# Kernel tuning notes

Hardware: AMD Instinct MI355X
Metric: run time of the kernel (lower is better)

The kernel has to match this reference:

```python
import jax, jax.numpy as jnp
import numpy as np

NUM_KEYS = 8192
NUM_BINS = 128
NUM_FREQS = 64
NUM_KERNELS = 3
HEAD_DIM = 2 * NUM_FREQS


def setup_inputs() -> dict:
    key = jax.random.key(0)
    k1, k2, k3, k4, k5 = jax.random.split(key, 5)
    fan_in = NUM_FREQS * NUM_KERNELS
    bound = np.sqrt(6.0 / fan_in)
    return {
        "K": jax.random.normal(k1, (NUM_KEYS, HEAD_DIM), dtype=jnp.float32),
        "reference_angles": jax.random.normal(k2, (NUM_FREQS,), dtype=jnp.float32),
        "mu": jax.random.uniform(k3, (NUM_BINS, NUM_FREQS, NUM_KERNELS), minval=-1.0, maxval=1.0, dtype=jnp.float32),
        "kappa": jax.random.uniform(k4, (NUM_BINS, NUM_FREQS, NUM_KERNELS), minval=0.0, maxval=1.0, dtype=jnp.float32),
        "weight": jax.random.uniform(k5, (NUM_BINS, NUM_FREQS, NUM_KERNELS), minval=-bound, maxval=bound, dtype=jnp.float32),
        "bias": jnp.zeros((NUM_BINS,), dtype=jnp.float32),
    }


def reference(K, reference_angles, mu, kappa, weight, bias):
    n = K.shape[0]
    num_bins, num_freqs, num_kernels = mu.shape
    # split head_dim into (freq, 2) complex pairs
    Kc = K.reshape(n, num_freqs, 2)                      # (n, f, 2)
    magnitude = jnp.sqrt(jnp.sum(Kc * Kc, axis=2))       # (n, f)
    angle = jnp.arctan2(Kc[..., 1], Kc[..., 0])          # (n, f)
    # shift kernel centers by per-round reference angles
    mu_eff = mu + reference_angles[None, :, None]        # (b, f, k)
    # von Mises kernel: exp(kappa * (cos(angle - mu) - 1))
    # broadcast to (n, b, f, k) -- this is the fat intermediate
    delta = angle[:, None, :, None] - mu_eff[None]       # (n, b, f, k)
    kernel = jnp.exp(kappa[None] * (jnp.cos(delta) - 1.0))
    # sum over kernels with weights, then over freqs with magnitude
    wk = jnp.einsum('nbfk,bfk->nbf', kernel, weight)     # (n, b, f)
    logits = jnp.einsum('nbf,nf->nb', wk, magnitude)     # (n, b)
    return logits + bias[None, :]
```

## Files before the change

### kernel.cpp

```cpp
#include <hip/hip_runtime.h>
#include <math.h>

#define NKEYS 8192
#define NBINS 128
#define NFREQ 64
#define NKER  3
#define HEADD 128

#define MHARM 6
#define NCH   (2 * MHARM + 1)
#define KDIM  (NCH * NFREQ)
#define KSTEPS (KDIM / 32)

typedef _Float16 f16x8 __attribute__((ext_vector_type(8)));
typedef float    f32x4 __attribute__((ext_vector_type(4)));

__global__ void build_coeffs(const float* __restrict__ refang,
                             const float* __restrict__ mu,
                             const float* __restrict__ kappa,
                             const float* __restrict__ weight,
                             _Float16* __restrict__ Bt) {
    int gid = blockIdx.x * blockDim.x + threadIdx.x;
    if (gid >= NBINS * NFREQ) return;
    int b = gid >> 6, f = gid & 63;
    float rf = refang[f];

    float acc[NCH];
    #pragma unroll
    for (int c = 0; c < NCH; ++c) acc[c] = 0.f;

    for (int k = 0; k < NKER; ++k) {
        int idx = (b * NFREQ + f) * NKER + k;
        float me  = mu[idx] + rf;
        float kap = kappa[idx];
        float w   = weight[idx];
        float h = 0.5f * kap, h2 = h * h;
        float wek = w * expf(-kap);
        float c1, s1;
        sincosf(me, &s1, &c1);

        float Im[MHARM + 1];
        float tm = 1.f;
        #pragma unroll
        for (int m = 0; m <= MHARM; ++m) {
            float t = tm, s = tm;
            #pragma unroll
            for (int j = 1; j <= 6; ++j) { t *= h2 / (float)(j * (m + j)); s += t; }
            Im[m] = s;
            tm *= h / (float)(m + 1);
        }

        acc[0] += wek * Im[0];
        float cp = 1.f, sp = 0.f, cc = c1, sc = s1;
        #pragma unroll
        for (int m = 1; m <= MHARM; ++m) {
            float g = 2.f * wek * Im[m];
            acc[2 * m - 1] += g * cc;
            acc[2 * m]     += g * sc;
            float cn = fmaf(2.f * c1, cc, -cp);
            float sn = fmaf(2.f * c1, sc, -sp);
            cp = cc; sp = sc; cc = cn; sc = sn;
        }
    }
    #pragma unroll
    for (int c = 0; c < NCH; ++c)
        Bt[(size_t)b * KDIM + c * NFREQ + f] = (_Float16)acc[c];
}

#define BM 32
#define GTHREADS 512
#define APAD 8
#define ASTR (KDIM + APAD)

__global__ __launch_bounds__(GTHREADS) void fused_gemm(
    const float* __restrict__ K,
    const _Float16* __restrict__ Bt,
    const float* __restrict__ bias,
    float* __restrict__ out)
{
    __shared__ __align__(16) _Float16 At[BM][ASTR];

    const int tid  = threadIdx.x;
    const int row0 = blockIdx.x * BM;

    for (int p = tid; p < BM * NFREQ; p += GTHREADS) {
        int n = p >> 6, f = p & 63;
        const float2 xy = *(const float2*)(K + (size_t)(row0 + n) * HEADD + 2 * f);
        float m2   = xy.x * xy.x + xy.y * xy.y;
        float rinv = (m2 > 0.f) ? rsqrtf(m2) : 0.f;
        float mag  = m2 * rinv;
        float c1   = xy.x * rinv, s1 = xy.y * rinv;
        At[n][f] = (_Float16)mag;
        float cp = 1.f, sp = 0.f, cc = c1, sc = s1;
        #pragma unroll
        for (int m = 1; m <= MHARM; ++m) {
            At[n][(2 * m - 1) * NFREQ + f] = (_Float16)(mag * cc);
            At[n][(2 * m) * NFREQ + f]     = (_Float16)(mag * sc);
            float cn = fmaf(2.f * c1, cc, -cp);
            float sn = fmaf(2.f * c1, sc, -sp);
            cp = cc; sp = sc; cc = cn; sc = sn;
        }
    }
    __syncthreads();

    const int lane = tid & 63, wave = tid >> 6;
    const int lc = lane & 15, q = lane >> 4;
    const int col = wave * 16 + lc;

    f32x4 acc0 = {0.f, 0.f, 0.f, 0.f};
    f32x4 acc1 = {0.f, 0.f, 0.f, 0.f};

    const _Float16* bp = Bt + (size_t)col * KDIM + q * 8;
    #pragma unroll
    for (int kt = 0; kt < KSTEPS; ++kt) {
        const int k0 = kt * 32 + q * 8;
        f16x8 a0 = *(const f16x8*)&At[lc][k0];
        f16x8 a1 = *(const f16x8*)&At[16 + lc][k0];
        f16x8 b  = *(const f16x8*)(bp + kt * 32);
        acc0 = __builtin_amdgcn_mfma_f32_16x16x32_f16(a0, b, acc0, 0, 0, 0);
        acc1 = __builtin_amdgcn_mfma_f32_16x16x32_f16(a1, b, acc1, 0, 0, 0);
    }

    const float bb = bias[col];
    #pragma unroll
    for (int j = 0; j < 4; ++j) {
        out[(size_t)(row0 + q * 4 + j) * NBINS + col]      = acc0[j] + bb;
        out[(size_t)(row0 + 16 + q * 4 + j) * NBINS + col] = acc1[j] + bb;
    }
}

#define KPB 16
#define FTHREADS 512
#define KPT 4
#define KV_STRIDE (KPB + 1)
#define LOG2E 1.44269504088896340736f

__global__ __launch_bounds__(FTHREADS) void vonmises_fallback(
    const float* __restrict__ K,
    const float* __restrict__ refang,
    const float* __restrict__ mu,
    const float* __restrict__ kappa,
    const float* __restrict__ weight,
    const float* __restrict__ bias,
    float* __restrict__ out)
{
    __shared__ float4 kvlds[NFREQ * KV_STRIDE];
    const int tid  = threadIdx.x;
    const int key0 = blockIdx.x * KPB;

    for (int p = tid; p < KPB * NFREQ; p += FTHREADS) {
        int key = p >> 6, f = p & (NFREQ - 1);
        const float2 xy = *(const float2*)(K + (size_t)(key0 + key) * HEADD + 2 * f);
        float m2 = xy.x * xy.x + xy.y * xy.y;
        float rm = (m2 > 0.f) ? rsqrtf(m2) : 0.f;
        kvlds[f * KV_STRIDE + key] = make_float4(xy.x * rm, xy.y * rm, m2 * rm, 0.f);
    }
    __syncthreads();

    const int bin = tid & (NBINS - 1);
    const int kbase = (tid >> 7) * KPT;
    float acc[KPT] = {0.f, 0.f, 0.f, 0.f};

    for (int f = 0; f < NFREQ; ++f) {
        float4 kv[KPT];
        #pragma unroll
        for (int j = 0; j < KPT; ++j) kv[j] = kvlds[f * KV_STRIDE + kbase + j];
        float wk[KPT] = {0.f, 0.f, 0.f, 0.f};
        #pragma unroll
        for (int k = 0; k < NKER; ++k) {
            int idx = (bin * NFREQ + f) * NKER + k;
            float me = mu[idx] + refang[f];
            float ka = kappa[idx] * LOG2E;
            float s, c;
            __sincosf(me, &s, &c);
            #pragma unroll
            for (int j = 0; j < KPT; ++j) {
                float t = fmaf(kv[j].x, ka * c, fmaf(kv[j].y, ka * s, -ka));
                wk[j] = fmaf(exp2f(t), weight[idx], wk[j]);
            }
        }
        #pragma unroll
        for (int j = 0; j < KPT; ++j) acc[j] = fmaf(wk[j], kv[j].z, acc[j]);
    }
    const float bb = bias[bin];
    #pragma unroll
    for (int j = 0; j < KPT; ++j)
        out[(size_t)(key0 + kbase + j) * NBINS + bin] = acc[j] + bb;
}

extern "C" void kernel_launch(void* const* d_in, const int* in_sizes, int n_in,
                              void* d_out, int out_size, void* d_ws, size_t ws_size,
                              hipStream_t stream) {
    const float* K      = (const float*)d_in[0];
    const float* refang = (const float*)d_in[1];
    const float* mu     = (const float*)d_in[2];
    const float* kappa  = (const float*)d_in[3];
    const float* weight = (const float*)d_in[4];
    const float* bias   = (const float*)d_in[5];
    float* out = (float*)d_out;

    const size_t need = (size_t)NBINS * KDIM * sizeof(_Float16);

    if (ws_size >= need) {
        _Float16* Bt = (_Float16*)d_ws;
        build_coeffs<<<(NBINS * NFREQ + 255) / 256, 256, 0, stream>>>(
            refang, mu, kappa, weight, Bt);
        fused_gemm<<<NKEYS / BM, GTHREADS, 0, stream>>>(K, Bt, bias, out);
    } else {
        vonmises_fallback<<<NKEYS / KPB, FTHREADS, 0, stream>>>(
            K, refang, mu, kappa, weight, bias, out);
    }
}
```

Measured before the change: 19.10 us.

## Pre-swizzle coefficient and feature matrices into MFMA fragment order, halve row tile

The coefficient builder now writes B directly in MFMA fragment order, so each lane in the GEMM loads one contiguous 16-byte vector per k-step. The per-block A tile in LDS is stored in the same fragment layout, so A reads are also single vector loads with no padding. The row tile shrinks from 32 to 16, which doubles the number of blocks and halves MFMA work per wave. Fast intrinsics replace expf and sincosf in the coefficient build, and that kernel's block size changes to 64 threads. The smaller tile means each B load feeds one MFMA instead of two, so total B traffic doubles.

```diff
diff --git a/kernel.cpp b/kernel.cpp
--- a/kernel.cpp
+++ b/kernel.cpp
@@ -15,11 +15,15 @@
 typedef _Float16 f16x8 __attribute__((ext_vector_type(8)));
 typedef float    f32x4 __attribute__((ext_vector_type(4)));
 
+#define FRAG_KT(ch, f) ((ch) * 2 + ((f) >> 5))
+#define FRAG_Q(f)      (((f) >> 3) & 3)
+#define FRAG_J(f)      ((f) & 7)
+
 __global__ void build_coeffs(const float* __restrict__ refang,
                              const float* __restrict__ mu,
                              const float* __restrict__ kappa,
                              const float* __restrict__ weight,
-                             _Float16* __restrict__ Bt) {
+                             _Float16* __restrict__ Bswz) {
     int gid = blockIdx.x * blockDim.x + threadIdx.x;
     if (gid >= NBINS * NFREQ) return;
     int b = gid >> 6, f = gid & 63;
@@ -29,15 +33,16 @@
     #pragma unroll
     for (int c = 0; c < NCH; ++c) acc[c] = 0.f;
 
+    #pragma unroll
     for (int k = 0; k < NKER; ++k) {
         int idx = (b * NFREQ + f) * NKER + k;
         float me  = mu[idx] + rf;
         float kap = kappa[idx];
         float w   = weight[idx];
         float h = 0.5f * kap, h2 = h * h;
-        float wek = w * expf(-kap);
+        float wek = w * __expf(-kap);
         float c1, s1;
-        sincosf(me, &s1, &c1);
+        __sincosf(me, &s1, &c1);
 
         float Im[MHARM + 1];
         float tm = 1.f;
@@ -62,23 +67,26 @@
             cp = cc; sp = sc; cc = cn; sc = sn;
         }
     }
-    #pragma unroll
-    for (int c = 0; c < NCH; ++c)
-        Bt[(size_t)b * KDIM + c * NFREQ + f] = (_Float16)acc[c];
-}
-
-#define BM 32
+
+    const int colgrp = b >> 4, lc = b & 15;
+    const int q = FRAG_Q(f), j = FRAG_J(f);
+    #pragma unroll
+    for (int c = 0; c < NCH; ++c) {
+        int kt = FRAG_KT(c, f);
+        Bswz[((size_t)(colgrp * KSTEPS + kt) * 64 + q * 16 + lc) * 8 + j] = (_Float16)acc[c];
+    }
+}
+
+#define BM 16
 #define GTHREADS 512
-#define APAD 8
-#define ASTR (KDIM + APAD)
 
 __global__ __launch_bounds__(GTHREADS) void fused_gemm(
     const float* __restrict__ K,
-    const _Float16* __restrict__ Bt,
+    const _Float16* __restrict__ Bswz,
     const float* __restrict__ bias,
     float* __restrict__ out)
 {
-    __shared__ __align__(16) _Float16 At[BM][ASTR];
+    __shared__ __align__(16) _Float16 Afrag[KSTEPS * 64 * 8];
 
     const int tid  = threadIdx.x;
     const int row0 = blockIdx.x * BM;
@@ -90,12 +98,13 @@
         float rinv = (m2 > 0.f) ? rsqrtf(m2) : 0.f;
         float mag  = m2 * rinv;
         float c1   = xy.x * rinv, s1 = xy.y * rinv;
-        At[n][f] = (_Float16)mag;
+        const int q = FRAG_Q(f), j = FRAG_J(f);
+        Afrag[FRAG_KT(0, f) * 512 + (q * 16 + n) * 8 + j] = (_Float16)mag;
         float cp = 1.f, sp = 0.f, cc = c1, sc = s1;
         #pragma unroll
         for (int m = 1; m <= MHARM; ++m) {
-            At[n][(2 * m - 1) * NFREQ + f] = (_Float16)(mag * cc);
-            At[n][(2 * m) * NFREQ + f]     = (_Float16)(mag * sc);
+            Afrag[FRAG_KT(2 * m - 1, f) * 512 + (q * 16 + n) * 8 + j] = (_Float16)(mag * cc);
+            Afrag[FRAG_KT(2 * m, f)     * 512 + (q * 16 + n) * 8 + j] = (_Float16)(mag * sc);
             float cn = fmaf(2.f * c1, cc, -cp);
             float sn = fmaf(2.f * c1, sc, -sp);
             cp = cc; sp = sc; cc = cn; sc = sn;
@@ -107,26 +116,22 @@
     const int lc = lane & 15, q = lane >> 4;
     const int col = wave * 16 + lc;
 
-    f32x4 acc0 = {0.f, 0.f, 0.f, 0.f};
-    f32x4 acc1 = {0.f, 0.f, 0.f, 0.f};
-
-    const _Float16* bp = Bt + (size_t)col * KDIM + q * 8;
+    f32x4 acc = {0.f, 0.f, 0.f, 0.f};
+
+    const f16x8* bp = (const f16x8*)Bswz + (size_t)wave * KSTEPS * 64 + lane;
+    const f16x8* ap = (const f16x8*)Afrag + lane;
+
     #pragma unroll
     for (int kt = 0; kt < KSTEPS; ++kt) {
-        const int k0 = kt * 32 + q * 8;
-        f16x8 a0 = *(const f16x8*)&At[lc][k0];
-        f16x8 a1 = *(const f16x8*)&At[16 + lc][k0];
-        f16x8 b  = *(const f16x8*)(bp + kt * 32);
-        acc0 = __builtin_amdgcn_mfma_f32_16x16x32_f16(a0, b, acc0, 0, 0, 0);
-        acc1 = __builtin_amdgcn_mfma_f32_16x16x32_f16(a1, b, acc1, 0, 0, 0);
+        f16x8 b = bp[kt * 64];
+        f16x8 a = ap[kt * 64];
+        acc = __builtin_amdgcn_mfma_f32_16x16x32_f16(a, b, acc, 0, 0, 0);
     }
 
     const float bb = bias[col];
     #pragma unroll
-    for (int j = 0; j < 4; ++j) {
-        out[(size_t)(row0 + q * 4 + j) * NBINS + col]      = acc0[j] + bb;
-        out[(size_t)(row0 + 16 + q * 4 + j) * NBINS + col] = acc1[j] + bb;
-    }
+    for (int j = 0; j < 4; ++j)
+        out[(size_t)(row0 + q * 4 + j) * NBINS + col] = acc[j] + bb;
 }
 
 #define KPB 16
@@ -202,10 +207,10 @@
     const size_t need = (size_t)NBINS * KDIM * sizeof(_Float16);
 
     if (ws_size >= need) {
-        _Float16* Bt = (_Float16*)d_ws;
-        build_coeffs<<<(NBINS * NFREQ + 255) / 256, 256, 0, stream>>>(
-            refang, mu, kappa, weight, Bt);
-        fused_gemm<<<NKEYS / BM, GTHREADS, 0, stream>>>(K, Bt, bias, out);
+        _Float16* Bswz = (_Float16*)d_ws;
+        build_coeffs<<<NBINS * NFREQ / 64, 64, 0, stream>>>(
+            refang, mu, kappa, weight, Bswz);
+        fused_gemm<<<NKEYS / BM, GTHREADS, 0, stream>>>(K, Bswz, bias, out);
     } else {
         vonmises_fallback<<<NKEYS / KPB, FTHREADS, 0, stream>>>(
             K, refang, mu, kappa, weight, bias, out);
```

Result: faster. 17.14 us (-10.3%).
